# Optimization experiments

Hardware: AMD Instinct MI355X
Metric: run time of the kernel (lower is better)

Reference implementation:

```python
import jax, jax.numpy as jnp
import numpy as np

N = 50000
E = 800000
D_IN = 128
D_HID = 512
D_OUT = 128
BN_EPS = 1e-5


def setup_inputs() -> dict:
    key = jax.random.key(0)
    ks = jax.random.split(key, 12)
    inp = {}
    inp["v"] = jax.random.normal(ks[0], (N, D_IN), dtype=jnp.float32)
    inp["src"] = jax.random.randint(ks[1], (E,), 0, N, dtype=jnp.int32)
    inp["dst"] = jax.random.randint(ks[2], (E,), 0, N, dtype=jnp.int32)
    inp["edge_weight"] = jax.random.uniform(ks[3], (E,), dtype=jnp.float32)
    # learned parameters
    inp["epsilon"] = jnp.zeros((1, 1), dtype=jnp.float32)  # nn.Parameter([[0.0]])
    s1 = 1.0 / np.sqrt(D_IN)
    s2 = 1.0 / np.sqrt(D_HID)
    inp["W1"] = jax.random.uniform(ks[4], (D_IN, D_HID), minval=-s1, maxval=s1, dtype=jnp.float32)
    inp["b1"] = jax.random.uniform(ks[5], (D_HID,), minval=-s1, maxval=s1, dtype=jnp.float32)
    inp["gamma1"] = jnp.ones((D_HID,), dtype=jnp.float32)
    inp["beta1"] = jnp.zeros((D_HID,), dtype=jnp.float32)
    inp["W2"] = jax.random.uniform(ks[6], (D_HID, D_OUT), minval=-s2, maxval=s2, dtype=jnp.float32)
    inp["b2"] = jax.random.uniform(ks[7], (D_OUT,), minval=-s2, maxval=s2, dtype=jnp.float32)
    inp["gamma2"] = jnp.ones((D_OUT,), dtype=jnp.float32)
    inp["beta2"] = jnp.zeros((D_OUT,), dtype=jnp.float32)
    return inp


def _batchnorm(x, gamma, beta):
    # training-mode BN: batch mean / biased variance over the node axis
    mean = jnp.mean(x, axis=0)
    var = jnp.mean(jnp.square(x - mean), axis=0)
    return gamma * (x - mean) * jax.lax.rsqrt(var + BN_EPS) + beta


def reference(v, src, dst, edge_weight, epsilon, W1, b1, gamma1, beta1, W2, b2, gamma2, beta2):
    n = v.shape[0]
    # sparse.mm(a, v): out[dst] += w * v[src]
    msgs = v[src] * edge_weight[:, None]               # [E, D_IN]
    v_agg = jax.ops.segment_sum(msgs, dst, num_segments=n)  # [N, D_IN]
    v_agg = v_agg + epsilon * v                        # epsilon residual
    h = jax.nn.relu(_batchnorm(v_agg @ W1 + b1, gamma1, beta1))
    out = jax.nn.relu(_batchnorm(h @ W2 + b2, gamma2, beta2))
    return out
```

## Files before the change

### kernel.cpp

```cpp
#include <hip/hip_runtime.h>

#define N_NODES 50000
#define E_EDGES 800000
#define D_INF   128
#define D_HIDF  512
#define D_OUTF  128
#define SCAN_NB ((N_NODES + 255) / 256)
#define MBLKS   ((N_NODES + 255) / 256)
#define EQ      (E_EDGES / 4)

typedef unsigned short u16;
typedef __attribute__((ext_vector_type(8))) short short8;
typedef __attribute__((ext_vector_type(4))) float floatx4;

__device__ __forceinline__ u16 f2bf(float f) {
    union { float f; unsigned u; } v; v.f = f;
    unsigned r = (v.u + 0x7fffu + ((v.u >> 16) & 1u)) >> 16;
    return (u16)r;
}
__device__ __forceinline__ float bf2f(u16 b) {
    union { unsigned u; float f; } v; v.u = ((unsigned)b) << 16; return v.f;
}

__global__ void cast_v_kernel(const float* __restrict__ v, u16* __restrict__ vbf) {
    int i = blockIdx.x * blockDim.x + threadIdx.x;
    if (i >= N_NODES * D_INF / 8) return;
    const float4 a = ((const float4*)v)[i * 2];
    const float4 b = ((const float4*)v)[i * 2 + 1];
    u16 o[8];
    o[0] = f2bf(a.x); o[1] = f2bf(a.y); o[2] = f2bf(a.z); o[3] = f2bf(a.w);
    o[4] = f2bf(b.x); o[5] = f2bf(b.y); o[6] = f2bf(b.z); o[7] = f2bf(b.w);
    ((float4*)vbf)[i] = *(const float4*)o;
}

__global__ void hist_kernel(const int* __restrict__ dst, int* __restrict__ counts,
                            int* __restrict__ pos) {
    int t = blockIdx.x * blockDim.x + threadIdx.x;
    if (t >= EQ) return;
    int d0 = dst[t];
    int d1 = dst[t + EQ];
    int d2 = dst[t + 2 * EQ];
    int d3 = dst[t + 3 * EQ];
    int p0 = atomicAdd(&counts[d0], 1);
    int p1 = atomicAdd(&counts[d1], 1);
    int p2 = atomicAdd(&counts[d2], 1);
    int p3 = atomicAdd(&counts[d3], 1);
    pos[t]          = p0;
    pos[t + EQ]     = p1;
    pos[t + 2 * EQ] = p2;
    pos[t + 3 * EQ] = p3;
}

__global__ void prep_weights_kernel(const float* __restrict__ W1, const float* __restrict__ W2,
                                    u16* __restrict__ W1t, u16* __restrict__ W2t) {
    int idx = blockIdx.x * blockDim.x + threadIdx.x;
    if (idx >= 128 * 512) return;
    int k1 = idx >> 9, n1 = idx & 511;
    W1t[n1 * 128 + k1] = f2bf(W1[idx]);
    int k2 = idx >> 7, n2 = idx & 127;
    W2t[n2 * 512 + k2] = f2bf(W2[idx]);
}

__global__ __launch_bounds__(256) void reduce_kernel(const int* __restrict__ counts,
                                                     int* __restrict__ block_sums) {
    __shared__ int lsum[4];
    int tid = threadIdx.x;
    int gid = blockIdx.x * 256 + tid;
    int s = (gid < N_NODES) ? counts[gid] : 0;
#pragma unroll
    for (int off = 32; off; off >>= 1) s += __shfl_down(s, off);
    if ((tid & 63) == 0) lsum[tid >> 6] = s;
    __syncthreads();
    if (tid == 0) block_sums[blockIdx.x] = lsum[0] + lsum[1] + lsum[2] + lsum[3];
}

__global__ __launch_bounds__(256) void scan_final(const int* __restrict__ counts,
                                                  const int* __restrict__ block_sums,
                                                  int* __restrict__ row_start) {
    __shared__ int sh[256];
    __shared__ int bs[256];
    int tid = threadIdx.x;
    int gid = blockIdx.x * 256 + tid;
    sh[tid] = (gid < N_NODES) ? counts[gid] : 0;
    bs[tid] = (tid < SCAN_NB) ? block_sums[tid] : 0;
    __syncthreads();
    for (int off = 1; off < 256; off <<= 1) {
        int t1 = (tid >= off) ? sh[tid - off] : 0;
        int t2 = (tid >= off) ? bs[tid - off] : 0;
        __syncthreads();
        sh[tid] += t1;
        bs[tid] += t2;
        __syncthreads();
    }
    int boff = (blockIdx.x == 0) ? 0 : bs[blockIdx.x - 1];
    int excl = (tid == 0) ? 0 : sh[tid - 1];
    if (gid < N_NODES) row_start[gid] = boff + excl;
    if (gid == 0) row_start[N_NODES] = E_EDGES;
}

__global__ void fill_kernel(const int* __restrict__ src, const int* __restrict__ dst,
                            const float* __restrict__ w, const int* __restrict__ pos,
                            const int* __restrict__ row_start,
                            int2* __restrict__ csr_ew) {
    int e = blockIdx.x * blockDim.x + threadIdx.x;
    if (e >= E_EDGES) return;
    int d = dst[e];
    int idx = row_start[d] + pos[e];
    int2 rec;
    rec.x = src[e];
    rec.y = __float_as_int(w[e]);
    csr_ew[idx] = rec;
}

__global__ __launch_bounds__(256) void gather_kernel(const u16* __restrict__ vbf,
                                                     const int* __restrict__ row_start,
                                                     const int2* __restrict__ csr_ew,
                                                     const float* __restrict__ eps_p,
                                                     u16* __restrict__ vagg) {
    int node = blockIdx.x * 16 + (threadIdx.x >> 4);
    if (node >= N_NODES) return;
    int c8 = (threadIdx.x & 15) << 3;
    int beg = row_start[node];
    int end = row_start[node + 1];
    float a[8] = {};
    int j = beg;
    for (; j + 1 < end; j += 2) {
        int2 e0 = csr_ew[j];
        int2 e1 = csr_ew[j + 1];
        float w0 = __int_as_float(e0.y);
        float w1 = __int_as_float(e1.y);
        float4 r0 = *(const float4*)(vbf + (size_t)e0.x * D_INF + c8);
        float4 r1 = *(const float4*)(vbf + (size_t)e1.x * D_INF + c8);
        const u16* p0 = (const u16*)&r0;
        const u16* p1 = (const u16*)&r1;
#pragma unroll
        for (int t = 0; t < 8; ++t) a[t] += w0 * bf2f(p0[t]);
#pragma unroll
        for (int t = 0; t < 8; ++t) a[t] += w1 * bf2f(p1[t]);
    }
    if (j < end) {
        int2 e0 = csr_ew[j];
        float w0 = __int_as_float(e0.y);
        float4 r0 = *(const float4*)(vbf + (size_t)e0.x * D_INF + c8);
        const u16* p0 = (const u16*)&r0;
#pragma unroll
        for (int t = 0; t < 8; ++t) a[t] += w0 * bf2f(p0[t]);
    }
    float e = eps_p[0];
    float4 rn = *(const float4*)(vbf + (size_t)node * D_INF + c8);
    const u16* pn = (const u16*)&rn;
    u16 o[8];
#pragma unroll
    for (int t = 0; t < 8; ++t) o[t] = f2bf(a[t] + e * bf2f(pn[t]));
    *(float4*)(vagg + (size_t)node * D_INF + c8) = *(const float4*)o;
}

template<int MT, int NT, int FUSE_A_BN>
__global__ __launch_bounds__(512) void mfma_gemm_bn(
        const u16* __restrict__ A, const u16* __restrict__ Bt,
        const float* __restrict__ bias,
        const float* __restrict__ a_scale, const float* __restrict__ a_shift,
        u16* __restrict__ Cout,
        float* __restrict__ psum, float* __restrict__ psq,
        int M, int Ncols, int K) {
    constexpr int NJ = NT / 32;
    constexpr int STG = (MT + NT) * 96;
    constexpr int SMEM_BYTES = (STG > 34816) ? STG : 34816;
    __shared__ __align__(16) char smem_raw[SMEM_BYTES];
    u16* As = (u16*)smem_raw;
    u16* Bs = As + MT * 48;
    const int bm = blockIdx.y * MT;
    const int bn = blockIdx.x * NT;
    const int tid = threadIdx.x;
    const int wave = tid >> 6, lane = tid & 63;
    const int wr = wave >> 1, wc = wave & 1;
    const int wm = wr * 64;
    const int wn = wc * (NT / 2);
    const int lm = lane & 15, quad = lane >> 4;

    floatx4 acc[4][NJ] = {};

    const int ksteps = K >> 5;
    for (int ks = 0; ks < ksteps; ++ks) {
        const int k0 = ks << 5;
        for (int c = tid; c < (MT + NT) * 4; c += 512) {
            int r = c >> 2;
            int kk = (c & 3) << 3;
            if (r < MT) {
                int row = bm + r;
                float4 av = make_float4(0.f, 0.f, 0.f, 0.f);
                if (row < M) {
                    av = *(const float4*)(A + (size_t)row * K + k0 + kk);
                    if (FUSE_A_BN) {
                        u16* ab = (u16*)&av;
                        const float4 s0 = *(const float4*)(a_scale + k0 + kk);
                        const float4 s1 = *(const float4*)(a_scale + k0 + kk + 4);
                        const float4 h0 = *(const float4*)(a_shift + k0 + kk);
                        const float4 h1 = *(const float4*)(a_shift + k0 + kk + 4);
                        ab[0] = f2bf(fmaxf(0.f, bf2f(ab[0]) * s0.x + h0.x));
                        ab[1] = f2bf(fmaxf(0.f, bf2f(ab[1]) * s0.y + h0.y));
                        ab[2] = f2bf(fmaxf(0.f, bf2f(ab[2]) * s0.z + h0.z));
                        ab[3] = f2bf(fmaxf(0.f, bf2f(ab[3]) * s0.w + h0.w));
                        ab[4] = f2bf(fmaxf(0.f, bf2f(ab[4]) * s1.x + h1.x));
                        ab[5] = f2bf(fmaxf(0.f, bf2f(ab[5]) * s1.y + h1.y));
                        ab[6] = f2bf(fmaxf(0.f, bf2f(ab[6]) * s1.z + h1.z));
                        ab[7] = f2bf(fmaxf(0.f, bf2f(ab[7]) * s1.w + h1.w));
                    }
                }
                *(float4*)&As[r * 48 + kk] = av;
            } else {
                int rb = r - MT;
                *(float4*)&Bs[rb * 48 + kk] =
                    *(const float4*)(Bt + (size_t)(bn + rb) * K + k0 + kk);
            }
        }
        __syncthreads();
        short8 af[4], bfr[NJ];
#pragma unroll
        for (int i = 0; i < 4; ++i)
            af[i] = *(const short8*)&As[(wm + i * 16 + lm) * 48 + quad * 8];
#pragma unroll
        for (int j = 0; j < NJ; ++j)
            bfr[j] = *(const short8*)&Bs[(wn + j * 16 + lm) * 48 + quad * 8];
#pragma unroll
        for (int i = 0; i < 4; ++i)
#pragma unroll
            for (int j = 0; j < NJ; ++j)
                acc[i][j] = __builtin_amdgcn_mfma_f32_16x16x32_bf16(af[i], bfr[j], acc[i][j], 0, 0, 0);
        __syncthreads();
    }

    float* redS = (float*)smem_raw;
    float* redQ = redS + NT;
    if (tid < NT) { redS[tid] = 0.f; redQ[tid] = 0.f; }
    __syncthreads();
    float bjv[NJ];
#pragma unroll
    for (int j = 0; j < NJ; ++j) {
        int cl = wn + j * 16 + lm;
        bjv[j] = bias[bn + cl];
        float s = 0.f, q = 0.f;
#pragma unroll
        for (int i = 0; i < 4; ++i) {
            int row0 = bm + wm + i * 16 + quad * 4;
#pragma unroll
            for (int r = 0; r < 4; ++r) {
                if (row0 + r < M) {
                    float x = acc[i][j][r] + bjv[j];
                    s += x; q += x * x;
                }
            }
        }
        s += __shfl_xor(s, 16); q += __shfl_xor(q, 16);
        s += __shfl_xor(s, 32); q += __shfl_xor(q, 32);
        if (quad == 0) {
            atomicAdd(&redS[cl], s);
            atomicAdd(&redQ[cl], q);
        }
    }
    __syncthreads();
    if (tid < NT) {
        psum[(size_t)blockIdx.y * Ncols + bn + tid] = redS[tid];
        psq [(size_t)blockIdx.y * Ncols + bn + tid] = redQ[tid];
    }

    float* obuf = (float*)smem_raw;
    constexpr int RH = MT / 128;
    constexpr int JH = NT / 64;
#pragma unroll
    for (int rh = 0; rh < RH; ++rh) {
#pragma unroll
        for (int jh = 0; jh < (JH ? JH : 1); ++jh) {
            __syncthreads();
            bool part = ((wr >> 1) == rh) && (NT == 64 || wc == jh);
            if (part) {
                int rbase = wm - rh * 128;
#pragma unroll
                for (int i = 0; i < 4; ++i)
#pragma unroll
                    for (int j = 0; j < NJ; ++j) {
                        int cp = (NT == 128) ? (j * 16 + lm) : (wn + j * 16 + lm);
#pragma unroll
                        for (int r = 0; r < 4; ++r)
                            obuf[(rbase + i * 16 + quad * 4 + r) * 68 + cp] =
                                acc[i][j][r] + bjv[j];
                    }
            }
            __syncthreads();
            int lr = tid >> 2;
            int seg = (tid & 3) << 4;
            int grow = bm + rh * 128 + lr;
            if (grow < M) {
                u16 ob[16];
#pragma unroll
                for (int t = 0; t < 4; ++t) {
                    float4 f = *(float4*)&obuf[lr * 68 + seg + t * 4];
                    ob[t * 4 + 0] = f2bf(f.x);
                    ob[t * 4 + 1] = f2bf(f.y);
                    ob[t * 4 + 2] = f2bf(f.z);
                    ob[t * 4 + 3] = f2bf(f.w);
                }
                u16* dstp = Cout + (size_t)grow * Ncols + bn + jh * 64 + seg;
                *(float4*)dstp       = *(float4*)(ob);
                *(float4*)(dstp + 8) = *(float4*)(ob + 8);
            }
        }
    }
}

__global__ __launch_bounds__(1024) void bn_finalize_kernel(
        const float* __restrict__ psum, const float* __restrict__ psq,
        const float* __restrict__ gamma, const float* __restrict__ beta,
        float* __restrict__ scale, float* __restrict__ shift,
        int nblocks, int Ncols, float inv_n) {
    __shared__ float shS[16][64];
    __shared__ float shQ[16][64];
    const int tx = threadIdx.x;
    const int ty = threadIdx.y;
    const int c = blockIdx.x * 64 + tx;
    float s = 0.f, q = 0.f;
    for (int b = ty; b < nblocks; b += 16) {
        s += psum[(size_t)b * Ncols + c];
        q += psq [(size_t)b * Ncols + c];
    }
    shS[ty][tx] = s;
    shQ[ty][tx] = q;
    __syncthreads();
    if (ty == 0) {
        float S = 0.f, Q = 0.f;
#pragma unroll
        for (int r = 0; r < 16; ++r) { S += shS[r][tx]; Q += shQ[r][tx]; }
        float m = S * inv_n;
        float var = Q * inv_n - m * m;
        float rs = rsqrtf(var + 1e-5f);
        float sc = gamma[c] * rs;
        scale[c] = sc;
        shift[c] = beta[c] - sc * m;
    }
}

__global__ void bn2_apply_kernel(const u16* __restrict__ X, float* __restrict__ Y,
                                 const float* __restrict__ scale,
                                 const float* __restrict__ shift, int n8) {
    int i = blockIdx.x * blockDim.x + threadIdx.x;
    if (i >= n8) return;
    int c = (i & 15) << 3;
    float4 raw = ((const float4*)X)[i];
    const u16* xb = (const u16*)&raw;
    float4 sc0 = *(const float4*)(scale + c);
    float4 sc1 = *(const float4*)(scale + c + 4);
    float4 sh0 = *(const float4*)(shift + c);
    float4 sh1 = *(const float4*)(shift + c + 4);
    float4 y0, y1;
    y0.x = fmaxf(0.f, bf2f(xb[0]) * sc0.x + sh0.x);
    y0.y = fmaxf(0.f, bf2f(xb[1]) * sc0.y + sh0.y);
    y0.z = fmaxf(0.f, bf2f(xb[2]) * sc0.z + sh0.z);
    y0.w = fmaxf(0.f, bf2f(xb[3]) * sc0.w + sh0.w);
    y1.x = fmaxf(0.f, bf2f(xb[4]) * sc1.x + sh1.x);
    y1.y = fmaxf(0.f, bf2f(xb[5]) * sc1.y + sh1.y);
    y1.z = fmaxf(0.f, bf2f(xb[6]) * sc1.z + sh1.z);
    y1.w = fmaxf(0.f, bf2f(xb[7]) * sc1.w + sh1.w);
    ((float4*)Y)[i * 2]     = y0;
    ((float4*)Y)[i * 2 + 1] = y1;
}

extern "C" void kernel_launch(void* const* d_in, const int* in_sizes, int n_in,
                              void* d_out, int out_size, void* d_ws, size_t ws_size,
                              hipStream_t stream) {
    const float* v    = (const float*)d_in[0];
    const int* src    = (const int*)d_in[1];
    const int* dst    = (const int*)d_in[2];
    const float* ew   = (const float*)d_in[3];
    const float* eps  = (const float*)d_in[4];
    const float* W1   = (const float*)d_in[5];
    const float* b1   = (const float*)d_in[6];
    const float* g1   = (const float*)d_in[7];
    const float* be1  = (const float*)d_in[8];
    const float* W2   = (const float*)d_in[9];
    const float* b2   = (const float*)d_in[10];
    const float* g2   = (const float*)d_in[11];
    const float* be2  = (const float*)d_in[12];
    float* out = (float*)d_out;

    char* base = (char*)d_ws;
    u16* x1   = (u16*)(base);
    u16* vbf  = (u16*)(base + 51200000ull);
    u16* vagg = (u16*)(base + 64000000ull);
    u16* x2   = (u16*)(base + 76800000ull);
    u16* W1t  = (u16*)(base + 89600000ull);
    u16* W2t  = (u16*)(base + 89731072ull);
    float* psum   = (float*)(base + 89862144ull);
    float* psq    = (float*)(base + 90663168ull);
    float* scale1 = (float*)(base + 91464192ull);
    float* shift1 = scale1 + 512;
    float* scale2 = shift1 + 512;
    float* shift2 = scale2 + 128;
    int* counts     = (int*)(shift2 + 128);
    int* row_start  = counts + 50000;
    int* pos        = row_start + 50004;
    int2* csr_ew    = (int2*)(pos + 800000);
    int* block_sums = (int*)(csr_ew + 800000);

    hipMemsetAsync(counts, 0, (size_t)50000 * sizeof(int), stream);

    cast_v_kernel<<<(N_NODES * D_INF / 8 + 255) / 256, 256, 0, stream>>>(v, vbf);
    hist_kernel<<<(EQ + 255) / 256, 256, 0, stream>>>(dst, counts, pos);
    prep_weights_kernel<<<(128 * 512 + 255) / 256, 256, 0, stream>>>(W1, W2, W1t, W2t);
    reduce_kernel<<<SCAN_NB, 256, 0, stream>>>(counts, block_sums);
    scan_final<<<SCAN_NB, 256, 0, stream>>>(counts, block_sums, row_start);
    fill_kernel<<<(E_EDGES + 255) / 256, 256, 0, stream>>>(src, dst, ew, pos, row_start, csr_ew);
    gather_kernel<<<(N_NODES + 15) / 16, 256, 0, stream>>>(vbf, row_start, csr_ew, eps, vagg);

    {
        dim3 grid(D_HIDF / 128, MBLKS);
        mfma_gemm_bn<256, 128, 0><<<grid, 512, 0, stream>>>(vagg, W1t, b1, nullptr, nullptr,
                                                            x1, psum, psq, N_NODES, D_HIDF, D_INF);
    }
    bn_finalize_kernel<<<D_HIDF / 64, dim3(64, 16), 0, stream>>>(
        psum, psq, g1, be1, scale1, shift1, MBLKS, D_HIDF, 1.0f / N_NODES);

    {
        dim3 grid(D_OUTF / 64, MBLKS);
        mfma_gemm_bn<256, 64, 1><<<grid, 512, 0, stream>>>(x1, W2t, b2, scale1, shift1,
                                                           x2, psum, psq, N_NODES, D_OUTF, D_HIDF);
    }
    bn_finalize_kernel<<<D_OUTF / 64, dim3(64, 16), 0, stream>>>(
        psum, psq, g2, be2, scale2, shift2, MBLKS, D_OUTF, 1.0f / N_NODES);

    {
        int n8 = N_NODES * D_OUTF / 8;
        bn2_apply_kernel<<<(n8 + 255) / 256, 256, 0, stream>>>(x2, out, scale2, shift2, n8);
    }
}
```

Measured before the change: 282.7 us.

## Fold BN1 scale into W2, prefetch GEMM tiles, retile second GEMM

The BN1 scale is folded into a rescaled W2 (W2 * scale1), so the second GEMM's A-staging applies only relu(x + shift/scale). The GEMM now register-prefetches the next k-step's global tile while the current one is in LDS, and can read B fragments straight from global memory. The LDS stride drops from 48 to 40. The second GEMM becomes a 64x128 tile with 256 threads, giving more blocks. The fold relies on scale1 being positive (gamma>0) and divides by scale, which changes relu semantics when gamma is negative and adds rounding error.

Measured after the change: 288.9 us. +2.2%, slower.

```diff
diff --git a/kernel.cpp b/kernel.cpp
--- a/kernel.cpp
+++ b/kernel.cpp
@@ -7,6 +7,7 @@
 #define D_OUTF  128
 #define SCAN_NB ((N_NODES + 255) / 256)
 #define MBLKS   ((N_NODES + 255) / 256)
+#define G2BLKS  ((N_NODES + 63) / 64)
 #define EQ      (E_EDGES / 4)
 
 typedef unsigned short u16;
@@ -51,14 +52,19 @@
     pos[t + 3 * EQ] = p3;
 }
 
-__global__ void prep_weights_kernel(const float* __restrict__ W1, const float* __restrict__ W2,
-                                    u16* __restrict__ W1t, u16* __restrict__ W2t) {
+__global__ void prep_w1_kernel(const float* __restrict__ W1, u16* __restrict__ W1t) {
     int idx = blockIdx.x * blockDim.x + threadIdx.x;
     if (idx >= 128 * 512) return;
     int k1 = idx >> 9, n1 = idx & 511;
     W1t[n1 * 128 + k1] = f2bf(W1[idx]);
+}
+
+__global__ void prep_w2_kernel(const float* __restrict__ W2, const float* __restrict__ scale1,
+                               u16* __restrict__ W2t) {
+    int idx = blockIdx.x * blockDim.x + threadIdx.x;
+    if (idx >= 512 * 128) return;
     int k2 = idx >> 7, n2 = idx & 127;
-    W2t[n2 * 512 + k2] = f2bf(W2[idx]);
+    W2t[n2 * 512 + k2] = f2bf(W2[idx] * scale1[k2]);
 }
 
 __global__ __launch_bounds__(256) void reduce_kernel(const int* __restrict__ counts,
@@ -155,78 +161,135 @@
     *(float4*)(vagg + (size_t)node * D_INF + c8) = *(const float4*)o;
 }
 
-template<int MT, int NT, int FUSE_A_BN>
-__global__ __launch_bounds__(512) void mfma_gemm_bn(
+template<int MT, int NT, int TH, int WRW, int FUSE, int BDIR>
+__global__ __launch_bounds__(TH) void mfma_gemm_bn(
         const u16* __restrict__ A, const u16* __restrict__ Bt,
         const float* __restrict__ bias,
-        const float* __restrict__ a_scale, const float* __restrict__ a_shift,
+        const float* __restrict__ a_shift,
         u16* __restrict__ Cout,
         float* __restrict__ psum, float* __restrict__ psq,
         int M, int Ncols, int K) {
-    constexpr int NJ = NT / 32;
-    constexpr int STG = (MT + NT) * 96;
-    constexpr int SMEM_BYTES = (STG > 34816) ? STG : 34816;
+    constexpr int WAVES = TH / 64;
+    constexpr int WCW = WAVES / WRW;
+    constexpr int WMS = MT / WRW;
+    constexpr int WNS = NT / WCW;
+    constexpr int MI = WMS / 16;
+    constexpr int NJ = WNS / 16;
+    constexpr int RP = TH / 4;
+    constexpr int RH = MT / RP;
+    constexpr int JH = NT / 64;
+    constexpr int STG = MT * 80 + (BDIR ? 0 : NT * 80);
+    constexpr int OBUF = RP * 68 * 4;
+    constexpr int SMEM_BYTES = (STG > OBUF) ? STG : OBUF;
     __shared__ __align__(16) char smem_raw[SMEM_BYTES];
     u16* As = (u16*)smem_raw;
-    u16* Bs = As + MT * 48;
+    u16* Bs = As + MT * 40;
     const int bm = blockIdx.y * MT;
     const int bn = blockIdx.x * NT;
     const int tid = threadIdx.x;
     const int wave = tid >> 6, lane = tid & 63;
-    const int wr = wave >> 1, wc = wave & 1;
-    const int wm = wr * 64;
-    const int wn = wc * (NT / 2);
+    const int wr = wave / WCW, wc = wave % WCW;
+    const int wm = wr * WMS;
+    const int wn = wc * WNS;
     const int lm = lane & 15, quad = lane >> 4;
 
-    floatx4 acc[4][NJ] = {};
+    floatx4 acc[MI][NJ] = {};
+
+    constexpr int UNITS = (MT + (BDIR ? 0 : NT)) * 4;
+    constexpr int NU = UNITS / TH;
+    static_assert(NU * TH == UNITS, "staging units must divide thread count");
 
     const int ksteps = K >> 5;
+
+    float4 areg[NU];
+#pragma unroll
+    for (int u = 0; u < NU; ++u) {
+        int c = tid + u * TH;
+        int r = c >> 2, kk = (c & 3) << 3;
+        float4 av = make_float4(0.f, 0.f, 0.f, 0.f);
+        if (r < MT) {
+            int row = bm + r;
+            if (row < M) av = *(const float4*)(A + (size_t)row * K + kk);
+        } else {
+            av = *(const float4*)(Bt + (size_t)(bn + r - MT) * K + kk);
+        }
+        areg[u] = av;
+    }
+    short8 bnext[BDIR ? NJ : 1];
+    if constexpr (BDIR) {
+#pragma unroll
+        for (int j = 0; j < NJ; ++j)
+            bnext[j] = *(const short8*)(Bt + (size_t)(bn + wn + j * 16 + lm) * K + quad * 8);
+    }
+
     for (int ks = 0; ks < ksteps; ++ks) {
         const int k0 = ks << 5;
-        for (int c = tid; c < (MT + NT) * 4; c += 512) {
-            int r = c >> 2;
-            int kk = (c & 3) << 3;
+#pragma unroll
+        for (int u = 0; u < NU; ++u) {
+            int c = tid + u * TH;
+            int r = c >> 2, kk = (c & 3) << 3;
+            float4 av = areg[u];
             if (r < MT) {
-                int row = bm + r;
-                float4 av = make_float4(0.f, 0.f, 0.f, 0.f);
-                if (row < M) {
-                    av = *(const float4*)(A + (size_t)row * K + k0 + kk);
-                    if (FUSE_A_BN) {
+                if constexpr (FUSE) {
+                    if (bm + r < M) {
                         u16* ab = (u16*)&av;
-                        const float4 s0 = *(const float4*)(a_scale + k0 + kk);
-                        const float4 s1 = *(const float4*)(a_scale + k0 + kk + 4);
                         const float4 h0 = *(const float4*)(a_shift + k0 + kk);
                         const float4 h1 = *(const float4*)(a_shift + k0 + kk + 4);
-                        ab[0] = f2bf(fmaxf(0.f, bf2f(ab[0]) * s0.x + h0.x));
-                        ab[1] = f2bf(fmaxf(0.f, bf2f(ab[1]) * s0.y + h0.y));
-                        ab[2] = f2bf(fmaxf(0.f, bf2f(ab[2]) * s0.z + h0.z));
-                        ab[3] = f2bf(fmaxf(0.f, bf2f(ab[3]) * s0.w + h0.w));
-                        ab[4] = f2bf(fmaxf(0.f, bf2f(ab[4]) * s1.x + h1.x));
-                        ab[5] = f2bf(fmaxf(0.f, bf2f(ab[5]) * s1.y + h1.y));
-                        ab[6] = f2bf(fmaxf(0.f, bf2f(ab[6]) * s1.z + h1.z));
-                        ab[7] = f2bf(fmaxf(0.f, bf2f(ab[7]) * s1.w + h1.w));
+                        ab[0] = f2bf(fmaxf(0.f, bf2f(ab[0]) + h0.x));
+                        ab[1] = f2bf(fmaxf(0.f, bf2f(ab[1]) + h0.y));
+                        ab[2] = f2bf(fmaxf(0.f, bf2f(ab[2]) + h0.z));
+                        ab[3] = f2bf(fmaxf(0.f, bf2f(ab[3]) + h0.w));
+                        ab[4] = f2bf(fmaxf(0.f, bf2f(ab[4]) + h1.x));
+                        ab[5] = f2bf(fmaxf(0.f, bf2f(ab[5]) + h1.y));
+                        ab[6] = f2bf(fmaxf(0.f, bf2f(ab[6]) + h1.z));
+                        ab[7] = f2bf(fmaxf(0.f, bf2f(ab[7]) + h1.w));
                     }
                 }
-                *(float4*)&As[r * 48 + kk] = av;
+                *(float4*)&As[r * 40 + kk] = av;
             } else {
-                int rb = r - MT;
-                *(float4*)&Bs[rb * 48 + kk] =
-                    *(const float4*)(Bt + (size_t)(bn + rb) * K + k0 + kk);
+                *(float4*)&Bs[(r - MT) * 40 + kk] = av;
             }
         }
+        if (ks + 1 < ksteps) {
+            const int k1 = k0 + 32;
+#pragma unroll
+            for (int u = 0; u < NU; ++u) {
+                int c = tid + u * TH;
+                int r = c >> 2, kk = (c & 3) << 3;
+                float4 av = make_float4(0.f, 0.f, 0.f, 0.f);
+                if (r < MT) {
+                    int row = bm + r;
+                    if (row < M) av = *(const float4*)(A + (size_t)row * K + k1 + kk);
+                } else {
+                    av = *(const float4*)(Bt + (size_t)(bn + r - MT) * K + k1 + kk);
+                }
+                areg[u] = av;
+            }
+        }
         __syncthreads();
-        short8 af[4], bfr[NJ];
-#pragma unroll
-        for (int i = 0; i < 4; ++i)
-            af[i] = *(const short8*)&As[(wm + i * 16 + lm) * 48 + quad * 8];
-#pragma unroll
-        for (int j = 0; j < NJ; ++j)
-            bfr[j] = *(const short8*)&Bs[(wn + j * 16 + lm) * 48 + quad * 8];
-#pragma unroll
-        for (int i = 0; i < 4; ++i)
+        short8 af[MI], bcur[NJ];
+#pragma unroll
+        for (int i = 0; i < MI; ++i)
+            af[i] = *(const short8*)&As[(wm + i * 16 + lm) * 40 + quad * 8];
+        if constexpr (BDIR) {
+#pragma unroll
+            for (int j = 0; j < NJ; ++j) bcur[j] = bnext[j];
+            if (ks + 1 < ksteps) {
+#pragma unroll
+                for (int j = 0; j < NJ; ++j)
+                    bnext[j] = *(const short8*)(Bt + (size_t)(bn + wn + j * 16 + lm) * K
+                                                + k0 + 32 + quad * 8);
+            }
+        } else {
 #pragma unroll
             for (int j = 0; j < NJ; ++j)
-                acc[i][j] = __builtin_amdgcn_mfma_f32_16x16x32_bf16(af[i], bfr[j], acc[i][j], 0, 0, 0);
+                bcur[j] = *(const short8*)&Bs[(wn + j * 16 + lm) * 40 + quad * 8];
+        }
+#pragma unroll
+        for (int i = 0; i < MI; ++i)
+#pragma unroll
+            for (int j = 0; j < NJ; ++j)
+                acc[i][j] = __builtin_amdgcn_mfma_f32_16x16x32_bf16(af[i], bcur[j], acc[i][j], 0, 0, 0);
         __syncthreads();
     }
 
@@ -241,7 +304,7 @@
         bjv[j] = bias[bn + cl];
         float s = 0.f, q = 0.f;
 #pragma unroll
-        for (int i = 0; i < 4; ++i) {
+        for (int i = 0; i < MI; ++i) {
             int row0 = bm + wm + i * 16 + quad * 4;
 #pragma unroll
             for (int r = 0; r < 4; ++r) {
@@ -265,21 +328,19 @@
     }
 
     float* obuf = (float*)smem_raw;
-    constexpr int RH = MT / 128;
-    constexpr int JH = NT / 64;
 #pragma unroll
     for (int rh = 0; rh < RH; ++rh) {
 #pragma unroll
-        for (int jh = 0; jh < (JH ? JH : 1); ++jh) {
+        for (int jh = 0; jh < JH; ++jh) {
             __syncthreads();
-            bool part = ((wr >> 1) == rh) && (NT == 64 || wc == jh);
+            bool part = ((wm / RP) == rh) && ((wn >> 6) == jh);
             if (part) {
-                int rbase = wm - rh * 128;
-#pragma unroll
-                for (int i = 0; i < 4; ++i)
+                int rbase = wm % RP;
+#pragma unroll
+                for (int i = 0; i < MI; ++i)
 #pragma unroll
                     for (int j = 0; j < NJ; ++j) {
-                        int cp = (NT == 128) ? (j * 16 + lm) : (wn + j * 16 + lm);
+                        int cp = (wn & 63) + j * 16 + lm;
 #pragma unroll
                         for (int r = 0; r < 4; ++r)
                             obuf[(rbase + i * 16 + quad * 4 + r) * 68 + cp] =
@@ -289,7 +350,7 @@
             __syncthreads();
             int lr = tid >> 2;
             int seg = (tid & 3) << 4;
-            int grow = bm + rh * 128 + lr;
+            int grow = bm + rh * RP + lr;
             if (grow < M) {
                 u16 ob[16];
 #pragma unroll
@@ -311,7 +372,7 @@
 __global__ __launch_bounds__(1024) void bn_finalize_kernel(
         const float* __restrict__ psum, const float* __restrict__ psq,
         const float* __restrict__ gamma, const float* __restrict__ beta,
-        float* __restrict__ scale, float* __restrict__ shift,
+        float* __restrict__ scale, float* __restrict__ shift, float* __restrict__ tshift,
         int nblocks, int Ncols, float inv_n) {
     __shared__ float shS[16][64];
     __shared__ float shQ[16][64];
@@ -334,8 +395,10 @@
         float var = Q * inv_n - m * m;
         float rs = rsqrtf(var + 1e-5f);
         float sc = gamma[c] * rs;
+        float sh = beta[c] - sc * m;
         scale[c] = sc;
-        shift[c] = beta[c] - sc * m;
+        shift[c] = sh;
+        if (tshift) tshift[c] = sh / sc;
     }
 }
 
@@ -395,7 +458,8 @@
     float* shift1 = scale1 + 512;
     float* scale2 = shift1 + 512;
     float* shift2 = scale2 + 128;
-    int* counts     = (int*)(shift2 + 128);
+    float* tshift1 = shift2 + 128;
+    int* counts     = (int*)(tshift1 + 512);
     int* row_start  = counts + 50000;
     int* pos        = row_start + 50004;
     int2* csr_ew    = (int2*)(pos + 800000);
@@ -405,7 +469,7 @@
 
     cast_v_kernel<<<(N_NODES * D_INF / 8 + 255) / 256, 256, 0, stream>>>(v, vbf);
     hist_kernel<<<(EQ + 255) / 256, 256, 0, stream>>>(dst, counts, pos);
-    prep_weights_kernel<<<(128 * 512 + 255) / 256, 256, 0, stream>>>(W1, W2, W1t, W2t);
+    prep_w1_kernel<<<(128 * 512 + 255) / 256, 256, 0, stream>>>(W1, W1t);
     reduce_kernel<<<SCAN_NB, 256, 0, stream>>>(counts, block_sums);
     scan_final<<<SCAN_NB, 256, 0, stream>>>(counts, block_sums, row_start);
     fill_kernel<<<(E_EDGES + 255) / 256, 256, 0, stream>>>(src, dst, ew, pos, row_start, csr_ew);
@@ -413,19 +477,21 @@
 
     {
         dim3 grid(D_HIDF / 128, MBLKS);
-        mfma_gemm_bn<256, 128, 0><<<grid, 512, 0, stream>>>(vagg, W1t, b1, nullptr, nullptr,
-                                                            x1, psum, psq, N_NODES, D_HIDF, D_INF);
+        mfma_gemm_bn<256, 128, 512, 4, 0, 0><<<grid, 512, 0, stream>>>(
+            vagg, W1t, b1, nullptr, x1, psum, psq, N_NODES, D_HIDF, D_INF);
     }
     bn_finalize_kernel<<<D_HIDF / 64, dim3(64, 16), 0, stream>>>(
-        psum, psq, g1, be1, scale1, shift1, MBLKS, D_HIDF, 1.0f / N_NODES);
+        psum, psq, g1, be1, scale1, shift1, tshift1, MBLKS, D_HIDF, 1.0f / N_NODES);
+
+    prep_w2_kernel<<<(512 * 128 + 255) / 256, 256, 0, stream>>>(W2, scale1, W2t);
 
     {
-        dim3 grid(D_OUTF / 64, MBLKS);
-        mfma_gemm_bn<256, 64, 1><<<grid, 512, 0, stream>>>(x1, W2t, b2, scale1, shift1,
-                                                           x2, psum, psq, N_NODES, D_OUTF, D_HIDF);
+        dim3 grid(1, G2BLKS);
+        mfma_gemm_bn<64, 128, 256, 1, 1, 1><<<grid, 256, 0, stream>>>(
+            x1, W2t, b2, tshift1, x2, psum, psq, N_NODES, D_OUTF, D_HIDF);
     }
     bn_finalize_kernel<<<D_OUTF / 64, dim3(64, 16), 0, stream>>>(
-        psum, psq, g2, be2, scale2, shift2, MBLKS, D_OUTF, 1.0f / N_NODES);
+        psum, psq, g2, be2, scale2, shift2, nullptr, G2BLKS, D_OUTF, 1.0f / N_NODES);
 
     {
         int n8 = N_NODES * D_OUTF / 8;
```

## Recompute GEMM1 in fused MLP kernel to avoid storing hidden activations

Applied to the files above, without the earlier changes.

The first GEMM now runs twice. A stats-only pass computes the BN1 sums without writing the 50000x512 hidden tensor, and a fused kernel recomputes GEMM1 per 64-row tile, applies BN1+ReLU in LDS and feeds GEMM2 directly. This removes the large bf16 x1 write and its re-read in exchange for doubling the GEMM1 FLOPs. LDS staging now uses global_load_lds with XOR swizzling, and the cast, weight-prep and histogram kernels are merged into one launch.

New measurement: 275.4 us. 1.03x faster.

```diff
diff --git a/kernel.cpp b/kernel.cpp
--- a/kernel.cpp
+++ b/kernel.cpp
@@ -6,12 +6,20 @@
 #define D_HIDF  512
 #define D_OUTF  128
 #define SCAN_NB ((N_NODES + 255) / 256)
-#define MBLKS   ((N_NODES + 255) / 256)
+#define M1BLKS  ((N_NODES + 255) / 256)
+#define FBLKS   ((N_NODES + 63) / 64)
 #define EQ      (E_EDGES / 4)
+
+#define CAST_NB  3125
+#define PREPW_NB 256
+#define HIST_NB  ((EQ + 255) / 256)
+#define PREP_ALL_NB (CAST_NB + 2 * PREPW_NB + HIST_NB)
 
 typedef unsigned short u16;
 typedef __attribute__((ext_vector_type(8))) short short8;
 typedef __attribute__((ext_vector_type(4))) float floatx4;
+typedef const __attribute__((address_space(1))) void gas_t;
+typedef __attribute__((address_space(3))) void las_t;
 
 __device__ __forceinline__ u16 f2bf(float f) {
     union { float f; unsigned u; } v; v.f = f;
@@ -22,43 +30,45 @@
     union { unsigned u; float f; } v; v.u = ((unsigned)b) << 16; return v.f;
 }
 
-__global__ void cast_v_kernel(const float* __restrict__ v, u16* __restrict__ vbf) {
-    int i = blockIdx.x * blockDim.x + threadIdx.x;
-    if (i >= N_NODES * D_INF / 8) return;
-    const float4 a = ((const float4*)v)[i * 2];
-    const float4 b = ((const float4*)v)[i * 2 + 1];
-    u16 o[8];
-    o[0] = f2bf(a.x); o[1] = f2bf(a.y); o[2] = f2bf(a.z); o[3] = f2bf(a.w);
-    o[4] = f2bf(b.x); o[5] = f2bf(b.y); o[6] = f2bf(b.z); o[7] = f2bf(b.w);
-    ((float4*)vbf)[i] = *(const float4*)o;
-}
-
-__global__ void hist_kernel(const int* __restrict__ dst, int* __restrict__ counts,
-                            int* __restrict__ pos) {
-    int t = blockIdx.x * blockDim.x + threadIdx.x;
-    if (t >= EQ) return;
-    int d0 = dst[t];
-    int d1 = dst[t + EQ];
-    int d2 = dst[t + 2 * EQ];
-    int d3 = dst[t + 3 * EQ];
-    int p0 = atomicAdd(&counts[d0], 1);
-    int p1 = atomicAdd(&counts[d1], 1);
-    int p2 = atomicAdd(&counts[d2], 1);
-    int p3 = atomicAdd(&counts[d3], 1);
-    pos[t]          = p0;
-    pos[t + EQ]     = p1;
-    pos[t + 2 * EQ] = p2;
-    pos[t + 3 * EQ] = p3;
-}
-
-__global__ void prep_weights_kernel(const float* __restrict__ W1, const float* __restrict__ W2,
-                                    u16* __restrict__ W1t, u16* __restrict__ W2t) {
-    int idx = blockIdx.x * blockDim.x + threadIdx.x;
-    if (idx >= 128 * 512) return;
-    int k1 = idx >> 9, n1 = idx & 511;
-    W1t[n1 * 128 + k1] = f2bf(W1[idx]);
-    int k2 = idx >> 7, n2 = idx & 127;
-    W2t[n2 * 512 + k2] = f2bf(W2[idx]);
+__global__ __launch_bounds__(256) void prep_all_kernel(
+        const float* __restrict__ v, const float* __restrict__ W1,
+        const float* __restrict__ W2, const int* __restrict__ dst,
+        u16* __restrict__ vbf, u16* __restrict__ W1t, u16* __restrict__ W2t,
+        int* __restrict__ counts, int* __restrict__ pos) {
+    int b = blockIdx.x;
+    int tid = threadIdx.x;
+    if (b < CAST_NB) {
+        int i = b * 256 + tid;
+        const float4 a = ((const float4*)v)[i * 2];
+        const float4 c = ((const float4*)v)[i * 2 + 1];
+        u16 o[8];
+        o[0] = f2bf(a.x); o[1] = f2bf(a.y); o[2] = f2bf(a.z); o[3] = f2bf(a.w);
+        o[4] = f2bf(c.x); o[5] = f2bf(c.y); o[6] = f2bf(c.z); o[7] = f2bf(c.w);
+        ((float4*)vbf)[i] = *(const float4*)o;
+    } else if (b < CAST_NB + PREPW_NB) {
+        int idx = (b - CAST_NB) * 256 + tid;
+        int k1 = idx >> 9, n1 = idx & 511;
+        W1t[n1 * 128 + k1] = f2bf(W1[idx]);
+    } else if (b < CAST_NB + 2 * PREPW_NB) {
+        int idx = (b - CAST_NB - PREPW_NB) * 256 + tid;
+        int k2 = idx >> 7, n2 = idx & 127;
+        W2t[n2 * 512 + k2] = f2bf(W2[idx]);
+    } else {
+        int t = (b - CAST_NB - 2 * PREPW_NB) * 256 + tid;
+        if (t >= EQ) return;
+        int d0 = dst[t];
+        int d1 = dst[t + EQ];
+        int d2 = dst[t + 2 * EQ];
+        int d3 = dst[t + 3 * EQ];
+        int p0 = atomicAdd(&counts[d0], 1);
+        int p1 = atomicAdd(&counts[d1], 1);
+        int p2 = atomicAdd(&counts[d2], 1);
+        int p3 = atomicAdd(&counts[d3], 1);
+        pos[t]          = p0;
+        pos[t + EQ]     = p1;
+        pos[t + 2 * EQ] = p2;
+        pos[t + 3 * EQ] = p3;
+    }
 }
 
 __global__ __launch_bounds__(256) void reduce_kernel(const int* __restrict__ counts,
@@ -155,155 +165,276 @@
     *(float4*)(vagg + (size_t)node * D_INF + c8) = *(const float4*)o;
 }
 
-template<int MT, int NT, int FUSE_A_BN>
-__global__ __launch_bounds__(512) void mfma_gemm_bn(
+__global__ __launch_bounds__(512) void stats_gemm1(
         const u16* __restrict__ A, const u16* __restrict__ Bt,
         const float* __restrict__ bias,
-        const float* __restrict__ a_scale, const float* __restrict__ a_shift,
-        u16* __restrict__ Cout,
-        float* __restrict__ psum, float* __restrict__ psq,
-        int M, int Ncols, int K) {
-    constexpr int NJ = NT / 32;
-    constexpr int STG = (MT + NT) * 96;
-    constexpr int SMEM_BYTES = (STG > 34816) ? STG : 34816;
-    __shared__ __align__(16) char smem_raw[SMEM_BYTES];
-    u16* As = (u16*)smem_raw;
-    u16* Bs = As + MT * 48;
-    const int bm = blockIdx.y * MT;
-    const int bn = blockIdx.x * NT;
+        float* __restrict__ psum, float* __restrict__ psq, int M) {
+    __shared__ __align__(16) char smem[24576];
+    u16* As = (u16*)smem;
+    u16* Bs = (u16*)(smem + 16384);
+    const int bm = blockIdx.y * 256;
+    const int bn = blockIdx.x * 128;
     const int tid = threadIdx.x;
     const int wave = tid >> 6, lane = tid & 63;
     const int wr = wave >> 1, wc = wave & 1;
-    const int wm = wr * 64;
-    const int wn = wc * (NT / 2);
+    const int wm = wr * 64, wn = wc * 64;
     const int lm = lane & 15, quad = lane >> 4;
-
-    floatx4 acc[4][NJ] = {};
-
-    const int ksteps = K >> 5;
-    for (int ks = 0; ks < ksteps; ++ks) {
+    floatx4 acc[4][4] = {};
+    for (int ks = 0; ks < 4; ++ks) {
         const int k0 = ks << 5;
-        for (int c = tid; c < (MT + NT) * 4; c += 512) {
-            int r = c >> 2;
-            int kk = (c & 3) << 3;
-            if (r < MT) {
-                int row = bm + r;
-                float4 av = make_float4(0.f, 0.f, 0.f, 0.f);
-                if (row < M) {
-                    av = *(const float4*)(A + (size_t)row * K + k0 + kk);
-                    if (FUSE_A_BN) {
-                        u16* ab = (u16*)&av;
-                        const float4 s0 = *(const float4*)(a_scale + k0 + kk);
-                        const float4 s1 = *(const float4*)(a_scale + k0 + kk + 4);
-                        const float4 h0 = *(const float4*)(a_shift + k0 + kk);
-                        const float4 h1 = *(const float4*)(a_shift + k0 + kk + 4);
-                        ab[0] = f2bf(fmaxf(0.f, bf2f(ab[0]) * s0.x + h0.x));
-                        ab[1] = f2bf(fmaxf(0.f, bf2f(ab[1]) * s0.y + h0.y));
-                        ab[2] = f2bf(fmaxf(0.f, bf2f(ab[2]) * s0.z + h0.z));
-                        ab[3] = f2bf(fmaxf(0.f, bf2f(ab[3]) * s0.w + h0.w));
-                        ab[4] = f2bf(fmaxf(0.f, bf2f(ab[4]) * s1.x + h1.x));
-                        ab[5] = f2bf(fmaxf(0.f, bf2f(ab[5]) * s1.y + h1.y));
-                        ab[6] = f2bf(fmaxf(0.f, bf2f(ab[6]) * s1.z + h1.z));
-                        ab[7] = f2bf(fmaxf(0.f, bf2f(ab[7]) * s1.w + h1.w));
-                    }
+        {
+            const int sub = lane >> 2, s = lane & 3;
+#pragma unroll
+            for (int t = 0; t < 3; ++t) {
+                int ch = wave * 3 + t;
+                if (ch < 16) {
+                    int row = ch * 16 + sub;
+                    int grow = bm + row; if (grow > M - 1) grow = M - 1;
+                    int ss = s ^ (row & 3);
+                    __builtin_amdgcn_global_load_lds(
+                        (gas_t*)(A + (size_t)grow * 128 + k0 + ss * 8),
+                        (las_t*)(As + row * 32 + s * 8), 16, 0, 0);
+                } else {
+                    int row = (ch - 16) * 16 + sub;
+                    int ss = s ^ (row & 3);
+                    __builtin_amdgcn_global_load_lds(
+                        (gas_t*)(Bt + (size_t)(bn + row) * 128 + k0 + ss * 8),
+                        (las_t*)(Bs + row * 32 + s * 8), 16, 0, 0);
                 }
-                *(float4*)&As[r * 48 + kk] = av;
-            } else {
-                int rb = r - MT;
-                *(float4*)&Bs[rb * 48 + kk] =
-                    *(const float4*)(Bt + (size_t)(bn + rb) * K + k0 + kk);
             }
         }
         __syncthreads();
-        short8 af[4], bfr[NJ];
+        short8 af[4], bfr[4];
+#pragma unroll
+        for (int i = 0; i < 4; ++i) {
+            int row = wm + i * 16 + lm;
+            af[i] = *(const short8*)&As[row * 32 + ((quad ^ (row & 3)) * 8)];
+        }
+#pragma unroll
+        for (int j = 0; j < 4; ++j) {
+            int row = wn + j * 16 + lm;
+            bfr[j] = *(const short8*)&Bs[row * 32 + ((quad ^ (row & 3)) * 8)];
+        }
 #pragma unroll
         for (int i = 0; i < 4; ++i)
-            af[i] = *(const short8*)&As[(wm + i * 16 + lm) * 48 + quad * 8];
-#pragma unroll
-        for (int j = 0; j < NJ; ++j)
-            bfr[j] = *(const short8*)&Bs[(wn + j * 16 + lm) * 48 + quad * 8];
-#pragma unroll
-        for (int i = 0; i < 4; ++i)
-#pragma unroll
-            for (int j = 0; j < NJ; ++j)
+#pragma unroll
+            for (int j = 0; j < 4; ++j)
                 acc[i][j] = __builtin_amdgcn_mfma_f32_16x16x32_bf16(af[i], bfr[j], acc[i][j], 0, 0, 0);
         __syncthreads();
     }
-
-    float* redS = (float*)smem_raw;
-    float* redQ = redS + NT;
-    if (tid < NT) { redS[tid] = 0.f; redQ[tid] = 0.f; }
-    __syncthreads();
-    float bjv[NJ];
-#pragma unroll
-    for (int j = 0; j < NJ; ++j) {
+    float* redS = (float*)smem;
+    float* redQ = redS + 128;
+    if (tid < 128) { redS[tid] = 0.f; redQ[tid] = 0.f; }
+    __syncthreads();
+#pragma unroll
+    for (int j = 0; j < 4; ++j) {
         int cl = wn + j * 16 + lm;
-        bjv[j] = bias[bn + cl];
+        float bj = bias[bn + cl];
         float s = 0.f, q = 0.f;
 #pragma unroll
         for (int i = 0; i < 4; ++i) {
             int row0 = bm + wm + i * 16 + quad * 4;
 #pragma unroll
-            for (int r = 0; r < 4; ++r) {
-                if (row0 + r < M) {
-                    float x = acc[i][j][r] + bjv[j];
-                    s += x; q += x * x;
-                }
-            }
+            for (int r = 0; r < 4; ++r)
+                if (row0 + r < M) { float x = acc[i][j][r] + bj; s += x; q += x * x; }
         }
         s += __shfl_xor(s, 16); q += __shfl_xor(q, 16);
         s += __shfl_xor(s, 32); q += __shfl_xor(q, 32);
-        if (quad == 0) {
-            atomicAdd(&redS[cl], s);
-            atomicAdd(&redQ[cl], q);
-        }
-    }
-    __syncthreads();
-    if (tid < NT) {
-        psum[(size_t)blockIdx.y * Ncols + bn + tid] = redS[tid];
-        psq [(size_t)blockIdx.y * Ncols + bn + tid] = redQ[tid];
-    }
-
-    float* obuf = (float*)smem_raw;
-    constexpr int RH = MT / 128;
-    constexpr int JH = NT / 64;
-#pragma unroll
-    for (int rh = 0; rh < RH; ++rh) {
-#pragma unroll
-        for (int jh = 0; jh < (JH ? JH : 1); ++jh) {
-            __syncthreads();
-            bool part = ((wr >> 1) == rh) && (NT == 64 || wc == jh);
-            if (part) {
-                int rbase = wm - rh * 128;
-#pragma unroll
-                for (int i = 0; i < 4; ++i)
-#pragma unroll
-                    for (int j = 0; j < NJ; ++j) {
-                        int cp = (NT == 128) ? (j * 16 + lm) : (wn + j * 16 + lm);
-#pragma unroll
-                        for (int r = 0; r < 4; ++r)
-                            obuf[(rbase + i * 16 + quad * 4 + r) * 68 + cp] =
-                                acc[i][j][r] + bjv[j];
-                    }
+        if (quad == 0) { atomicAdd(&redS[cl], s); atomicAdd(&redQ[cl], q); }
+    }
+    __syncthreads();
+    if (tid < 128) {
+        psum[(size_t)blockIdx.y * 512 + bn + tid] = redS[tid];
+        psq [(size_t)blockIdx.y * 512 + bn + tid] = redQ[tid];
+    }
+}
+
+__global__ __launch_bounds__(512, 4) void fused_mlp(
+        const u16* __restrict__ vagg, const u16* __restrict__ W1t,
+        const u16* __restrict__ W2t,
+        const float* __restrict__ b1, const float* __restrict__ scale1,
+        const float* __restrict__ shift1, const float* __restrict__ b2,
+        u16* __restrict__ x2, float* __restrict__ psum, float* __restrict__ psq,
+        int M) {
+    __shared__ __align__(16) char smem[81920];
+    u16* As  = (u16*)smem;
+    u16* W1s = (u16*)(smem + 16384);
+    u16* W2s = (u16*)smem;
+    u16* hs  = (u16*)(smem + 16384);
+    const int bm = blockIdx.x * 64;
+    const int tid = threadIdx.x;
+    const int wave = tid >> 6, lane = tid & 63;
+    const int wr = wave >> 2, wc = wave & 3;
+    const int wm = wr * 32;
+    const int wn1 = wc * 128;
+    const int wn2 = wc * 32;
+    const int lm = lane & 15, quad = lane >> 4;
+
+    floatx4 acc1[2][8] = {};
+    floatx4 acc2[2][2] = {};
+
+    auto stage_w1 = [&](int win) {
+#pragma unroll
+        for (int u = 0; u < 8; ++u) {
+            int c = tid + u * 512;
+            int col = c >> 3, s = c & 7;
+            __builtin_amdgcn_global_load_lds(
+                (gas_t*)(W1t + (size_t)col * 128 + win * 64 + ((s ^ (col & 7)) * 8)),
+                (las_t*)(W1s + col * 64 + s * 8), 16, 0, 0);
+        }
+    };
+    auto stage_w2 = [&](int win) {
+#pragma unroll
+        for (int u = 0; u < 2; ++u) {
+            int c = tid + u * 512;
+            int n = c >> 3, s = c & 7;
+            __builtin_amdgcn_global_load_lds(
+                (gas_t*)(W2t + (size_t)n * 512 + win * 64 + ((s ^ (n & 7)) * 8)),
+                (las_t*)(W2s + n * 64 + s * 8), 16, 0, 0);
+        }
+    };
+    auto compute1 = [&](int ks) {
+        short8 a[2], b[8];
+#pragma unroll
+        for (int i = 0; i < 2; ++i) {
+            int row = wm + i * 16 + lm;
+            a[i] = *(const short8*)&As[row * 128 + (((ks * 4 + quad) ^ (row & 7)) * 8)];
+        }
+#pragma unroll
+        for (int j = 0; j < 8; ++j) {
+            int col = wn1 + j * 16 + lm;
+            b[j] = *(const short8*)&W1s[col * 64 + ((((ks & 1) * 4 + quad) ^ (col & 7)) * 8)];
+        }
+#pragma unroll
+        for (int i = 0; i < 2; ++i)
+#pragma unroll
+            for (int j = 0; j < 8; ++j)
+                acc1[i][j] = __builtin_amdgcn_mfma_f32_16x16x32_bf16(a[i], b[j], acc1[i][j], 0, 0, 0);
+    };
+    auto compute2 = [&](int ks) {
+        short8 a[2], b[2];
+#pragma unroll
+        for (int i = 0; i < 2; ++i) {
+            int row = wm + i * 16 + lm;
+            a[i] = *(const short8*)&hs[row * 512 + (((ks * 4 + quad) ^ (row & 7)) * 8)];
+        }
+#pragma unroll
+        for (int j = 0; j < 2; ++j) {
+            int n = wn2 + j * 16 + lm;
+            b[j] = *(const short8*)&W2s[n * 64 + ((((ks & 1) * 4 + quad) ^ (n & 7)) * 8)];
+        }
+#pragma unroll
+        for (int i = 0; i < 2; ++i)
+#pragma unroll
+            for (int j = 0; j < 2; ++j)
+                acc2[i][j] = __builtin_amdgcn_mfma_f32_16x16x32_bf16(a[i], b[j], acc2[i][j], 0, 0, 0);
+    };
+
+#pragma unroll
+    for (int u = 0; u < 2; ++u) {
+        int c = tid + u * 512;
+        int row = c >> 4, s = c & 15;
+        int grow = bm + row; if (grow > M - 1) grow = M - 1;
+        __builtin_amdgcn_global_load_lds(
+            (gas_t*)(vagg + (size_t)grow * 128 + ((s ^ (row & 7)) * 8)),
+            (las_t*)(As + row * 128 + s * 8), 16, 0, 0);
+    }
+    stage_w1(0);
+    __syncthreads();
+    compute1(0); compute1(1);
+    __syncthreads();
+    stage_w1(1);
+    __syncthreads();
+    compute1(2); compute1(3);
+    __syncthreads();
+
+    stage_w2(0);
+    {
+        float hsc[8], hsh[8];
+#pragma unroll
+        for (int j = 0; j < 8; ++j) {
+            int col = wn1 + j * 16 + lm;
+            float sc = scale1[col];
+            hsc[j] = sc;
+            hsh[j] = shift1[col] + sc * b1[col];
+        }
+#pragma unroll
+        for (int i = 0; i < 2; ++i)
+#pragma unroll
+            for (int j = 0; j < 8; ++j)
+#pragma unroll
+                for (int r = 0; r < 4; ++r) {
+                    int row = wm + i * 16 + quad * 4 + r;
+                    int col = wn1 + j * 16 + lm;
+                    float hv = fmaxf(0.f, acc1[i][j][r] * hsc[j] + hsh[j]);
+                    hs[row * 512 + (((col >> 3) ^ (row & 7)) * 8) + (col & 7)] = f2bf(hv);
+                }
+    }
+    __syncthreads();
+
+#pragma unroll
+    for (int win = 0; win < 8; ++win) {
+        compute2(win * 2); compute2(win * 2 + 1);
+        __syncthreads();
+        if (win < 7) { stage_w2(win + 1); __syncthreads(); }
+    }
+
+    float* redS = (float*)smem;
+    float* redQ = redS + 128;
+    if (tid < 128) { redS[tid] = 0.f; redQ[tid] = 0.f; }
+    __syncthreads();
+    float bj2[2];
+#pragma unroll
+    for (int j = 0; j < 2; ++j) {
+        int cl = wn2 + j * 16 + lm;
+        bj2[j] = b2[cl];
+        float s = 0.f, q = 0.f;
+#pragma unroll
+        for (int i = 0; i < 2; ++i) {
+            int row0 = bm + wm + i * 16 + quad * 4;
+#pragma unroll
+            for (int r = 0; r < 4; ++r)
+                if (row0 + r < M) { float x = acc2[i][j][r] + bj2[j]; s += x; q += x * x; }
+        }
+        s += __shfl_xor(s, 16); q += __shfl_xor(q, 16);
+        s += __shfl_xor(s, 32); q += __shfl_xor(q, 32);
+        if (quad == 0) { atomicAdd(&redS[cl], s); atomicAdd(&redQ[cl], q); }
+    }
+    __syncthreads();
+    if (tid < 128) {
+        psum[(size_t)blockIdx.x * 128 + tid] = redS[tid];
+        psq [(size_t)blockIdx.x * 128 + tid] = redQ[tid];
+    }
+    __syncthreads();
+
+    float* obuf = (float*)smem;
+#pragma unroll
+    for (int i = 0; i < 2; ++i)
+#pragma unroll
+        for (int j = 0; j < 2; ++j)
+#pragma unroll
+            for (int r = 0; r < 4; ++r) {
+                int row = wm + i * 16 + quad * 4 + r;
+                int col = wn2 + j * 16 + lm;
+                obuf[row * 132 + col] = acc2[i][j][r] + bj2[j];
             }
-            __syncthreads();
-            int lr = tid >> 2;
-            int seg = (tid & 3) << 4;
-            int grow = bm + rh * 128 + lr;
-            if (grow < M) {
-                u16 ob[16];
-#pragma unroll
-                for (int t = 0; t < 4; ++t) {
-                    float4 f = *(float4*)&obuf[lr * 68 + seg + t * 4];
-                    ob[t * 4 + 0] = f2bf(f.x);
-                    ob[t * 4 + 1] = f2bf(f.y);
-                    ob[t * 4 + 2] = f2bf(f.z);
-                    ob[t * 4 + 3] = f2bf(f.w);
-                }
-                u16* dstp = Cout + (size_t)grow * Ncols + bn + jh * 64 + seg;
-                *(float4*)dstp       = *(float4*)(ob);
-                *(float4*)(dstp + 8) = *(float4*)(ob + 8);
+    __syncthreads();
+    {
+        int row = tid >> 3, seg = (tid & 7) * 16;
+        int grow = bm + row;
+        if (grow < M) {
+            u16 ob[16];
+#pragma unroll
+            for (int t = 0; t < 4; ++t) {
+                float4 f = *(float4*)&obuf[row * 132 + seg + t * 4];
+                ob[t * 4 + 0] = f2bf(f.x);
+                ob[t * 4 + 1] = f2bf(f.y);
+                ob[t * 4 + 2] = f2bf(f.z);
+                ob[t * 4 + 3] = f2bf(f.w);
             }
+            u16* dp = x2 + (size_t)grow * 128 + seg;
+            *(float4*)dp       = *(float4*)ob;
+            *(float4*)(dp + 8) = *(float4*)(ob + 8);
         }
     }
 }
@@ -383,7 +514,6 @@
     float* out = (float*)d_out;
 
     char* base = (char*)d_ws;
-    u16* x1   = (u16*)(base);
     u16* vbf  = (u16*)(base + 51200000ull);
     u16* vagg = (u16*)(base + 64000000ull);
     u16* x2   = (u16*)(base + 76800000ull);
@@ -403,29 +533,24 @@
 
     hipMemsetAsync(counts, 0, (size_t)50000 * sizeof(int), stream);
 
-    cast_v_kernel<<<(N_NODES * D_INF / 8 + 255) / 256, 256, 0, stream>>>(v, vbf);
-    hist_kernel<<<(EQ + 255) / 256, 256, 0, stream>>>(dst, counts, pos);
-    prep_weights_kernel<<<(128 * 512 + 255) / 256, 256, 0, stream>>>(W1, W2, W1t, W2t);
+    prep_all_kernel<<<PREP_ALL_NB, 256, 0, stream>>>(v, W1, W2, dst, vbf, W1t, W2t,
+                                                     counts, pos);
     reduce_kernel<<<SCAN_NB, 256, 0, stream>>>(counts, block_sums);
     scan_final<<<SCAN_NB, 256, 0, stream>>>(counts, block_sums, row_start);
     fill_kernel<<<(E_EDGES + 255) / 256, 256, 0, stream>>>(src, dst, ew, pos, row_start, csr_ew);
     gather_kernel<<<(N_NODES + 15) / 16, 256, 0, stream>>>(vbf, row_start, csr_ew, eps, vagg);
 
     {
-        dim3 grid(D_HIDF / 128, MBLKS);
-        mfma_gemm_bn<256, 128, 0><<<grid, 512, 0, stream>>>(vagg, W1t, b1, nullptr, nullptr,
-                                                            x1, psum, psq, N_NODES, D_HIDF, D_INF);
+        dim3 grid(D_HIDF / 128, M1BLKS);
+        stats_gemm1<<<grid, 512, 0, stream>>>(vagg, W1t, b1, psum, psq, N_NODES);
     }
     bn_finalize_kernel<<<D_HIDF / 64, dim3(64, 16), 0, stream>>>(
-        psum, psq, g1, be1, scale1, shift1, MBLKS, D_HIDF, 1.0f / N_NODES);
-
-    {
-        dim3 grid(D_OUTF / 64, MBLKS);
-        mfma_gemm_bn<256, 64, 1><<<grid, 512, 0, stream>>>(x1, W2t, b2, scale1, shift1,
-                                                           x2, psum, psq, N_NODES, D_OUTF, D_HIDF);
-    }
+        psum, psq, g1, be1, scale1, shift1, M1BLKS, D_HIDF, 1.0f / N_NODES);
+
+    fused_mlp<<<FBLKS, 512, 0, stream>>>(vagg, W1t, W2t, b1, scale1, shift1, b2,
+                                         x2, psum, psq, N_NODES);
     bn_finalize_kernel<<<D_OUTF / 64, dim3(64, 16), 0, stream>>>(
-        psum, psq, g2, be2, scale2, shift2, MBLKS, D_OUTF, 1.0f / N_NODES);
+        psum, psq, g2, be2, scale2, shift2, FBLKS, D_OUTF, 1.0f / N_NODES);
 
     {
         int n8 = N_NODES * D_OUTF / 8;
```
